# Kernel optimization log

Measured on AMD Instinct MI355X. Metric: run time of the kernel, lower is better.

The kernel has to match this reference:

```python
import jax, jax.numpy as jnp
import numpy as np

B, V, NX, R, D, H = 512, 2, 1024, 64, 512, 8
S, NC, HS = 4, 2, 64           # bc_state_dim, num_controls, state-branch hidden
FIN = S * HS + 128             # fusion input dim (state feats + control feats)


def _ln(x, g, b, eps=1e-5):
    mu = jnp.mean(x, axis=-1, keepdims=True)
    var = jnp.mean((x - mu) ** 2, axis=-1, keepdims=True)
    return (x - mu) * jax.lax.rsqrt(var + eps) * g + b


def setup_inputs() -> dict:
    key = jax.random.key(0)
    ks = iter(jax.random.split(key, 64))
    def rn(shape, s=0.02):
        return jax.random.normal(next(ks), shape, dtype=jnp.float32) * s
    inp = {}
    inp['a_n'] = jax.random.normal(next(ks), (B, V, R), dtype=jnp.float32)
    inp['BC_Ctrl'] = jax.random.normal(next(ks), (B, S + NC), dtype=jnp.float32)
    inp['Phi'] = rn((V, NX, R), 1.0 / np.sqrt(NX).astype(np.float32))
    # per-variable attention params (stacked on leading V axis)
    inp['Wq_w'] = rn((V, 1, D));   inp['Wq_b'] = rn((V, D))
    inp['Wk_w'] = rn((V, NX, D));  inp['Wk_b'] = rn((V, D))
    inp['Wv_w'] = rn((V, NX, D));  inp['Wv_b'] = rn((V, D))
    inp['attn_ow'] = rn((V, D, D)); inp['attn_ob'] = rn((V, D))
    inp['proj_w'] = rn((V, D, 1));  inp['proj_b'] = rn((V, 1))
    # ImprovedUpdateFFN (num_layers=3, hidden=d_model) + LayerNorm
    inp['ffn_w1'] = rn((V, R, D)); inp['ffn_b1'] = rn((V, D))
    inp['ffn_w2'] = rn((V, D, D)); inp['ffn_b2'] = rn((V, D))
    inp['ffn_w3'] = rn((V, D, R)); inp['ffn_b3'] = rn((V, R))
    inp['ffn_ln_g'] = jnp.ones((V, R), jnp.float32)
    inp['ffn_ln_b'] = jnp.zeros((V, R), jnp.float32)
    # a0_mapping: Linear -> ReLU -> LayerNorm
    inp['a0_w'] = rn((V, R, R)); inp['a0_b'] = rn((V, R))
    inp['a0_ln_g'] = jnp.ones((V, R), jnp.float32)
    inp['a0_ln_b'] = jnp.zeros((V, R), jnp.float32)
    inp['alpha'] = jnp.full((V,), 0.1, jnp.float32)
    # UniversalLifting params
    inp['sb_w'] = rn((S, 1, HS)); inp['sb_b'] = rn((S, HS))
    inp['cm_w1'] = rn((NC, 64));  inp['cm_b1'] = rn((64,))
    inp['cm_w2'] = rn((64, 128)); inp['cm_b2'] = rn((128,))
    inp['fu_w1'] = rn((FIN, 256)); inp['fu_b1'] = rn((256,))
    inp['fu_w2'] = rn((256, 512)); inp['fu_b2'] = rn((512,))
    inp['fu_w3'] = rn((512, 256)); inp['fu_b3'] = rn((256,))
    inp['fu_w4'] = rn((256, V * NX)); inp['fu_b4'] = rn((V * NX,))
    return inp


def reference(a_n, BC_Ctrl, Phi, Wq_w, Wq_b, Wk_w, Wk_b, Wv_w, Wv_b,
              attn_ow, attn_ob, proj_w, proj_b,
              ffn_w1, ffn_b1, ffn_w2, ffn_b2, ffn_w3, ffn_b3, ffn_ln_g, ffn_ln_b,
              a0_w, a0_b, a0_ln_g, a0_ln_b, alpha,
              sb_w, sb_b, cm_w1, cm_b1, cm_w2, cm_b2,
              fu_w1, fu_b1, fu_w2, fu_b2, fu_w3, fu_b3, fu_w4, fu_b4):
    gelu = jax.nn.gelu
    # ---- UniversalLifting: U_B [B, V, NX] ----
    bs = BC_Ctrl[:, :S]                                              # [B,S]
    sf = gelu(bs[:, :, None] * sb_w[None, :, 0, :] + sb_b[None])     # [B,S,HS]
    sf = sf.reshape(bs.shape[0], S * HS)
    cf = gelu(BC_Ctrl[:, S:] @ cm_w1 + cm_b1)
    cf = gelu(cf @ cm_w2 + cm_b2)
    f = jnp.concatenate([sf, cf], axis=-1)                           # [B,FIN]
    h = gelu(f @ fu_w1 + fu_b1)
    h = gelu(h @ fu_w2 + fu_b2)
    h = gelu(h @ fu_w3 + fu_b3)
    U_B = (h @ fu_w4 + fu_b4).reshape(-1, V, NX)
    # ---- a0 mapping: Linear -> ReLU -> LayerNorm ----
    a_map = jax.nn.relu(jnp.einsum('bvr,vrs->bvs', a_n, a0_w) + a0_b[None])
    a_map = _ln(a_map, a0_ln_g[None], a0_ln_b[None])                 # [B,V,R]
    # ---- ImprovedUpdateFFN residual update ----
    h1 = gelu(jnp.einsum('bvr,vrd->bvd', a_map, ffn_w1) + ffn_b1[None])
    h2 = gelu(jnp.einsum('bvd,vde->bve', h1, ffn_w2) + ffn_b2[None])
    o = jnp.einsum('bvd,vdr->bvr', h2, ffn_w3) + ffn_b3[None]
    ffn_update = _ln(o + a_map, ffn_ln_g[None], ffn_ln_b[None])      # [B,V,R]
    # ---- Q/K/V; K,V depend only on Phi (batch-independent) ----
    Q = a_map[:, :, :, None] * Wq_w[:, 0][None, :, None, :] + Wq_b[None, :, None, :]  # [B,V,R,D]
    K = jnp.einsum('vnr,vnd->vrd', Phi, Wk_w) + Wk_b[:, None, :]     # [V,R,D]
    Vm = jnp.einsum('vnr,vnd->vrd', Phi, Wv_w) + Wv_b[:, None, :]    # [V,R,D]
    hd = D // H
    Qh = Q.reshape(-1, V, R, H, hd)
    Kh = K.reshape(V, R, H, hd)
    Vh = Vm.reshape(V, R, H, hd)
    # softmax-free linear attention: z = Q (K^T V) per head
    KV = jnp.einsum('vrhk,vrhl->vhkl', Kh, Vh)                        # [V,H,hd,hd]
    z = jnp.einsum('bvrhk,vhkl->bvrhl', Qh, KV).reshape(-1, V, R, D)
    z = jnp.einsum('bvrd,vde->bvre', z, attn_ow) + attn_ob[None, :, None, :]
    z = z / jnp.sqrt(jnp.float32(D))
    a_update = jnp.einsum('bvrd,vdo->bvro', z, proj_w)[..., 0] + proj_b[:, 0][None, :, None]
    a_next = a_map + a_update + alpha[None, :, None] * ffn_update     # [B,V,R]
    U_hat = jnp.einsum('vnr,bvr->bvn', Phi, a_next) + U_B             # [B,V,NX]
    return U_hat
```

## Files before the change

kernel.cpp:

```cpp
#include <hip/hip_runtime.h>
#include <hip/hip_bf16.h>
#include <math.h>


typedef unsigned short ushort_t;
using short8 = __attribute__((ext_vector_type(8))) short;
using f32x4  = __attribute__((ext_vector_type(4))) float;

__device__ __forceinline__ float gelu_f(float x) {
    float x3 = x*x*x;
    return 0.5f*x*(1.0f + tanhf(0.7978845608028654f*(x + 0.044715f*x3)));
}

__device__ __forceinline__ float wave_sum(float x) {
    #pragma unroll
    for (int m = 32; m >= 1; m >>= 1) x += __shfl_xor(x, m, 64);
    return x;
}

__device__ __forceinline__ ushort_t f2bf(float x) {
    unsigned u = __float_as_uint(x);
    unsigned r = (u + 0x7FFFu + ((u >> 16) & 1u)) >> 16;
    return (ushort_t)r;
}
__device__ __forceinline__ float bf2f(ushort_t h) {
    return __uint_as_float(((unsigned)h) << 16);
}

struct Ptrs {
    const float *a_n, *BC, *Phi, *Wq_w, *Wq_b, *Wk_w, *Wk_b, *Wv_w, *Wv_b,
                *attn_ow, *attn_ob, *proj_w, *proj_b,
                *ffn_w3, *ffn_b3, *ffn_ln_g, *ffn_ln_b,
                *a0_w, *a0_b, *a0_ln_g, *a0_ln_b, *alpha,
                *sb_w, *sb_b, *cm_w1, *cm_b1, *cm_w2, *cm_b2,
                *fu_b1, *fu_b2, *fu_b3, *fu_b4, *ffn_b1, *ffn_b2;
    float *opj, *u0, *u1, *u2, *pkq, *pqq, *pvo, *phirs, *bias2, *out;
    ushort_t *amap_bf, *h1_bf, *h2_bf, *fbuf_bf, *hA_bf, *hB_bf;
    ushort_t *w_fu1t, *w_fu2t, *w_fu3t, *w_ffn1t, *w_ffn2t, *w_ffn3t,
             *Abig, *Bbig;
};

struct CvtDesc { const float* src; ushort_t* dst; int K, N, mode, ldd, coff; };
struct CvtArgs { CvtDesc d[12]; int cum[13]; };

__device__ void cvt_dev(char* smem, int tile, const CvtDesc& d, const Ptrs& p)
{
    const int t = threadIdx.x;
    if (d.mode == 2) {
        const int row = t >> 2, q = t & 3;
        const float* s = d.src + (long)(tile*64 + row)*64 + q*16;
        ushort_t* dst  = d.dst + (long)(tile*64 + row)*384 + d.coff + q*16;
        ushort_t* dz   = d.dst + (long)(tile*64 + row)*384 + (64 - d.coff) + q*16;
        float sum = 0.f;
        #pragma unroll
        for (int i = 0; i < 4; ++i) {
            float4 x = *(const float4*)(s + i*4);
            ushort4 w; w.x=f2bf(x.x); w.y=f2bf(x.y); w.z=f2bf(x.z); w.w=f2bf(x.w);
            *(ushort4*)(dst + i*4) = w;
            ushort4 z; z.x=0; z.y=0; z.z=0; z.w=0;
            *(ushort4*)(dz + i*4) = z;
            sum += x.x + x.y + x.z + x.w;
        }
        sum += __shfl_xor(sum, 1, 64);
        sum += __shfl_xor(sum, 2, 64);
        if (q == 0) p.phirs[d.K + tile*64 + row] = sum;
    } else {
        float* tl = (float*)smem;
        const int ntn = d.N >> 5;
        const int kt = tile / ntn, nt = tile % ntn;
        const int r = t >> 3, c0 = (t & 7) * 4;
        float4 v = *(const float4*)(d.src + (long)(kt*32 + r)*d.N + nt*32 + c0);
        tl[r*33 + c0] = v.x; tl[r*33 + c0+1] = v.y;
        tl[r*33 + c0+2] = v.z; tl[r*33 + c0+3] = v.w;
        __syncthreads();
        ushort4 w;
        w.x = f2bf(tl[(c0+0)*33 + r]); w.y = f2bf(tl[(c0+1)*33 + r]);
        w.z = f2bf(tl[(c0+2)*33 + r]); w.w = f2bf(tl[(c0+3)*33 + r]);
        *(ushort4*)(d.dst + (long)(nt*32 + r)*d.ldd + d.coff + kt*32 + c0) = w;
    }
}

__device__ void bgemm_dev(char* smem_,
    const ushort_t* __restrict__ A, const ushort_t* __restrict__ B,
    const float* __restrict__ bias,
    void* __restrict__ Cv, int m0, int n0, int K, int ldc,
    int EPI, bool OUTBF)
{
    ushort_t* lds = (ushort_t*)smem_;
    const int tid = threadIdx.x;
    const int w = tid >> 6, l = tid & 63;
    const int ml = l & 15, kg = l >> 4;
    const int srow = tid >> 2, sslot = tid & 3;
    const ushort_t* Ag = A + (long)(m0 + srow)*K + sslot*8;
    const ushort_t* Bg = B + (long)(n0 + srow)*K + sslot*8;
    auto L = [&](int buf, int ab, int row, int col) {
        return lds + (((buf*2 + ab)*64 + row)*40 + col);
    };
    f32x4 acc[4] = {};
    const int nt = K >> 5;
    int4 ra = *(const int4*)Ag;
    int4 rb = *(const int4*)Bg;
    *(int4*)L(0,0,srow,sslot*8) = ra;
    *(int4*)L(0,1,srow,sslot*8) = rb;
    __syncthreads();
    for (int t = 0; t < nt; ++t) {
        const int cur = t & 1;
        if (t + 1 < nt) {
            ra = *(const int4*)(Ag + (t+1)*32);
            rb = *(const int4*)(Bg + (t+1)*32);
        }
        short8 af = *(const short8*)L(cur,0,w*16 + ml,kg*8);
        #pragma unroll
        for (int f = 0; f < 4; ++f) {
            short8 bfr = *(const short8*)L(cur,1,f*16 + ml,kg*8);
            acc[f] = __builtin_amdgcn_mfma_f32_16x16x32_bf16(af, bfr, acc[f], 0, 0, 0);
        }
        if (t + 1 < nt) {
            *(int4*)L(cur^1,0,srow,sslot*8) = ra;
            *(int4*)L(cur^1,1,srow,sslot*8) = rb;
            __syncthreads();
        }
    }
    float* Cf = (float*)Cv; ushort_t* Cb = (ushort_t*)Cv;
    const int mr = m0 + w*16 + kg*4;
    const int nc = n0 + ml;
    #pragma unroll
    for (int f = 0; f < 4; ++f) {
        const int n = nc + f*16;
        const float bs = bias[n];
        #pragma unroll
        for (int r = 0; r < 4; ++r) {
            float x = acc[f][r] + bs;
            if (EPI == 1) x = gelu_f(x);
            if (OUTBF) Cb[(long)(mr + r)*ldc + n] = f2bf(x);
            else       Cf[(long)(mr + r)*ldc + n] = x;
        }
    }
}

__device__ void control_dev(char* smem, int b, const Ptrs& p)
{
    float* bc  = (float*)smem;
    float* cf1 = bc + 8;
    const int tid = threadIdx.x;
    if (tid < 6) bc[tid] = p.BC[b*6 + tid];
    __syncthreads();
    {
        int s = tid >> 6;
        p.fbuf_bf[(long)b*384 + tid] = f2bf(gelu_f(bc[s]*p.sb_w[tid] + p.sb_b[tid]));
    }
    if (tid < 64) {
        cf1[tid] = gelu_f(bc[4]*p.cm_w1[tid] + bc[5]*p.cm_w1[64+tid] + p.cm_b1[tid]);
    }
    __syncthreads();
    if (tid < 128) {
        float acc = p.cm_b2[tid];
        #pragma unroll 8
        for (int i = 0; i < 64; ++i) acc = fmaf(cf1[i], p.cm_w2[i*128 + tid], acc);
        p.fbuf_bf[(long)b*384 + 256 + tid] = f2bf(gelu_f(acc));
    }
}

__device__ void a_map_dev(char* smem, int bx, int v, const Ptrs& p)
{
    float* arow = (float*)smem;
    const int w = threadIdx.x >> 6, lane = threadIdx.x & 63;
    const int b = bx*4 + w;
    arow[w*64 + lane] = p.a_n[((long)b*2 + v)*64 + lane];
    __syncthreads();
    float acc = p.a0_b[v*64 + lane];
    #pragma unroll 8
    for (int rp = 0; rp < 64; ++rp)
        acc = fmaf(arow[w*64 + rp], p.a0_w[((long)v*64 + rp)*64 + lane], acc);
    float x = fmaxf(acc, 0.0f);
    float mu = wave_sum(x) * (1.0f/64.0f);
    float d = x - mu;
    float var = wave_sum(d*d) * (1.0f/64.0f);
    float y = d * rsqrtf(var + 1e-5f) * p.a0_ln_g[v*64 + lane] + p.a0_ln_b[v*64 + lane];
    p.amap_bf[((long)v*512 + b)*64 + lane] = f2bf(y);
}

__device__ void opj_dev(int oi, const Ptrs& p)
{
    const int tid = threadIdx.x;
    const int v = oi >> 3, dc = oi & 7;
    const int d = dc*64 + (tid >> 2);
    const int e0 = (tid & 3)*128;
    const float* row = p.attn_ow + ((long)v*512 + d)*512 + e0;
    const float* pj  = p.proj_w + v*512 + e0;
    float s = 0.f;
    #pragma unroll 8
    for (int j = 0; j < 128; ++j) s = fmaf(row[j], pj[j], s);
    s += __shfl_xor(s, 1, 64);
    s += __shfl_xor(s, 2, 64);
    if ((tid & 3) == 0) p.opj[v*512 + d] = s;
}

__device__ void u01_dev(int i, const Ptrs& p)
{
    const int tid = threadIdx.x;
    const int w = tid >> 6, lane = tid & 63;
    const int v = i >> 4, c = i & 15;
    const float* wq = p.Wq_w + v*512;
    const float* wb = p.Wq_b + v*512;
    for (int pass = 0; pass < 16; ++pass) {
        const int n = c*64 + pass*4 + w;
        const float* row = p.Wk_w + ((long)v*1024 + n)*512 + lane*8;
        float4 a = *(const float4*)row, b = *(const float4*)(row + 4);
        float s0 = 0.f, s1 = 0.f;
        #pragma unroll
        for (int j = 0; j < 8; ++j) {
            float x = (j < 4) ? ((const float*)&a)[j] : ((const float*)&b)[j-4];
            s0 = fmaf(x, wq[lane*8 + j], s0);
            s1 = fmaf(x, wb[lane*8 + j], s1);
        }
        s0 += __shfl_xor(s0,1,64); s0 += __shfl_xor(s0,2,64); s0 += __shfl_xor(s0,4,64);
        s1 += __shfl_xor(s1,1,64); s1 += __shfl_xor(s1,2,64); s1 += __shfl_xor(s1,4,64);
        if ((lane & 7) == 0) {
            const int h = lane >> 3;
            p.u0[((long)v*1024 + n)*8 + h] = s0;
            p.u1[((long)v*1024 + n)*8 + h] = s1;
        }
    }
}

__device__ void u2_dev(int i, const Ptrs& p)
{
    const int tid = threadIdx.x;
    const int w = tid >> 6, lane = tid & 63;
    const int v = i >> 4, c = i & 15;
    const float* oj = p.opj + v*512;
    for (int pass = 0; pass < 16; ++pass) {
        const int n = c*64 + pass*4 + w;
        const float* row = p.Wv_w + ((long)v*1024 + n)*512 + lane*8;
        float4 a = *(const float4*)row, b = *(const float4*)(row + 4);
        float s0 = 0.f;
        #pragma unroll
        for (int j = 0; j < 8; ++j) {
            float x = (j < 4) ? ((const float*)&a)[j] : ((const float*)&b)[j-4];
            s0 = fmaf(x, oj[lane*8 + j], s0);
        }
        s0 += __shfl_xor(s0,1,64); s0 += __shfl_xor(s0,2,64); s0 += __shfl_xor(s0,4,64);
        if ((lane & 7) == 0) p.u2[((long)v*1024 + n)*8 + (lane >> 3)] = s0;
    }
}

__device__ void kqqq_dev(int i, const Ptrs& p)
{
    const int tid = threadIdx.x;
    const int v = i >> 3, c = i & 7;
    const int r = tid & 63, hp = tid >> 6;
    const int h0 = hp*2, h1 = h0 + 1;
    float k0=0.f,k1=0.f,q0=0.f,q1=0.f;
    const float* Pb = p.Phi + ((long)v*1024 + c*128)*64 + r;
    const float* U0 = p.u0 + ((long)v*1024 + c*128)*8;
    const float* U1 = p.u1 + ((long)v*1024 + c*128)*8;
    #pragma unroll 4
    for (int n = 0; n < 128; ++n) {
        float phi = Pb[(long)n*64];
        k0 = fmaf(phi, U0[n*8+h0], k0); k1 = fmaf(phi, U0[n*8+h1], k1);
        q0 = fmaf(phi, U1[n*8+h0], q0); q1 = fmaf(phi, U1[n*8+h1], q1);
    }
    const long o = (((long)v*8 + c)*64 + r)*8;
    p.pkq[o+h0] = k0; p.pkq[o+h1] = k1;
    p.pqq[o+h0] = q0; p.pqq[o+h1] = q1;
}

__device__ void pvo_dev(int i, const Ptrs& p)
{
    const int tid = threadIdx.x;
    const int v = i >> 3, c = i & 7;
    const int r = tid & 63, hp = tid >> 6;
    const int h0 = hp*2, h1 = h0 + 1;
    float a0 = 0.f, a1 = 0.f;
    const float* Pb = p.Phi + ((long)v*1024 + c*128)*64 + r;
    const float* U2 = p.u2 + ((long)v*1024 + c*128)*8;
    #pragma unroll 4
    for (int n = 0; n < 128; ++n) {
        float phi = Pb[(long)n*64];
        a0 = fmaf(phi, U2[n*8+h0], a0);
        a1 = fmaf(phi, U2[n*8+h1], a1);
    }
    const long o = (((long)v*8 + c)*64 + r)*8;
    p.pvo[o+h0] = a0; p.pvo[o+h1] = a1;
}

__device__ float2 consts_final_dev(char* smem, int v, const Ptrs& p)
{
    const int tid = threadIdx.x;
    const int r = tid & 63, hp = tid >> 6;
    const int h0 = hp*2, h1 = h0 + 1;
    float k0=0.f,k1=0.f,q0=0.f,q1=0.f,w0=0.f,w1=0.f;
    #pragma unroll
    for (int c = 0; c < 8; ++c) {
        const long o = (((long)v*8 + c)*64 + r)*8;
        k0 += p.pkq[o+h0]; k1 += p.pkq[o+h1];
        q0 += p.pqq[o+h0]; q1 += p.pqq[o+h1];
        w0 += p.pvo[o+h0]; w1 += p.pvo[o+h1];
    }
    float bk0=0.f,bk1=0.f,bq0=0.f,bq1=0.f,bv0=0.f,bv1=0.f;
    #pragma unroll 8
    for (int j = 0; j < 64; ++j) {
        float b0 = p.Wk_b[v*512 + h0*64 + j], b1 = p.Wk_b[v*512 + h1*64 + j];
        bk0 = fmaf(b0, p.Wq_w[v*512 + h0*64 + j], bk0);
        bk1 = fmaf(b1, p.Wq_w[v*512 + h1*64 + j], bk1);
        bq0 = fmaf(b0, p.Wq_b[v*512 + h0*64 + j], bq0);
        bq1 = fmaf(b1, p.Wq_b[v*512 + h1*64 + j], bq1);
        float c0v = p.Wv_b[v*512 + h0*64 + j], c1v = p.Wv_b[v*512 + h1*64 + j];
        bv0 = fmaf(c0v, p.opj[v*512 + h0*64 + j], bv0);
        bv1 = fmaf(c1v, p.opj[v*512 + h1*64 + j], bv1);
    }
    w0 += bv0; w1 += bv1;
    k0 += bk0; k1 += bk1; q0 += bq0; q1 += bq1;
    float s1 = k0*w0 + k1*w1;
    float s0 = q0*w0 + q1*w1;
    float sA = p.attn_ob[v*512 + tid]*p.proj_w[v*512 + tid]
             + p.attn_ob[v*512 + 256 + tid]*p.proj_w[v*512 + 256 + tid];
    s1 = wave_sum(s1); s0 = wave_sum(s0); sA = wave_sum(sA);
    float* red = (float*)smem;
    const int w = tid >> 6, l = tid & 63;
    __syncthreads();
    if (l == 0) { red[w] = s1; red[4+w] = s0; red[8+w] = sA; }
    __syncthreads();
    float S1 = red[0]+red[1]+red[2]+red[3];
    float S0 = red[4]+red[5]+red[6]+red[7];
    float SA = red[8]+red[9]+red[10]+red[11];
    __syncthreads();
    const float inv = 0.044194173824159216f;
    float2 res;
    res.x = S1*inv;
    res.y = (S0 + SA)*inv + p.proj_b[v];
    return res;
}

__device__ void ogemm_ln_dev(char* smem_, int v, int m0, const Ptrs& p)
{
    const float c1 = consts_final_dev(smem_, v, p).x;

    ushort_t* lds = (ushort_t*)smem_;
    const int tid = threadIdx.x;
    const int w = tid >> 6, l = tid & 63;
    const int ml = l & 15, kg = l >> 4;
    const int srow = tid >> 2, sslot = tid & 3;
    const ushort_t* A = p.h2_bf + (long)v*262144;
    const ushort_t* B = p.w_ffn3t + (long)v*32768;
    const float* bias = p.ffn_b3 + v*64;
    const ushort_t* Ag = A + (long)(m0 + srow)*512 + sslot*8;
    const ushort_t* Bg = B + (long)srow*512 + sslot*8;
    auto L = [&](int buf, int ab, int row, int col) {
        return lds + (((buf*2 + ab)*64 + row)*40 + col);
    };
    f32x4 acc[4] = {};
    int4 ra = *(const int4*)Ag;
    int4 rb = *(const int4*)Bg;
    *(int4*)L(0,0,srow,sslot*8) = ra;
    *(int4*)L(0,1,srow,sslot*8) = rb;
    __syncthreads();
    for (int t = 0; t < 16; ++t) {
        const int cur = t & 1;
        if (t + 1 < 16) {
            ra = *(const int4*)(Ag + (t+1)*32);
            rb = *(const int4*)(Bg + (t+1)*32);
        }
        short8 af = *(const short8*)L(cur,0,w*16 + ml,kg*8);
        #pragma unroll
        for (int f = 0; f < 4; ++f) {
            short8 bfr = *(const short8*)L(cur,1,f*16 + ml,kg*8);
            acc[f] = __builtin_amdgcn_mfma_f32_16x16x32_bf16(af, bfr, acc[f], 0, 0, 0);
        }
        if (t + 1 < 16) {
            *(int4*)L(cur^1,0,srow,sslot*8) = ra;
            *(int4*)L(cur^1,1,srow,sslot*8) = rb;
            __syncthreads();
        }
    }
    __syncthreads();
    float* ot = (float*)smem_;
    {
        const int rl = w*16 + kg*4;
        #pragma unroll
        for (int f = 0; f < 4; ++f) {
            const int n = ml + f*16;
            const float bs = bias[n];
            #pragma unroll
            for (int r = 0; r < 4; ++r)
                ot[(rl + r)*66 + n] = acc[f][r] + bs;
        }
    }
    __syncthreads();
    const float g  = p.ffn_ln_g[v*64 + l];
    const float bt = p.ffn_ln_b[v*64 + l];
    const float al = p.alpha[v];
    for (int rr = 0; rr < 16; ++rr) {
        const int row = w*16 + rr;
        const int b = m0 + row;
        const float am = bf2f(p.amap_bf[((long)v*512 + b)*64 + l]);
        float t = ot[row*66 + l] + am;
        float mu = wave_sum(t) * (1.0f/64.0f);
        float dd = t - mu;
        float var = wave_sum(dd*dd) * (1.0f/64.0f);
        float u = dd * rsqrtf(var + 1e-5f) * g + bt;
        p.Abig[(long)b*384 + v*64 + l] = f2bf(am*(1.0f + c1) + al*u);
    }
}

__device__ void bias2_dev(char* smem, const Ptrs& p)
{
    const float c00 = consts_final_dev(smem, 0, p).y;
    const float c01 = consts_final_dev(smem, 1, p).y;
    #pragma unroll
    for (int k = 0; k < 8; ++k) {
        const int n2 = k*256 + threadIdx.x;
        const float c0 = (n2 >> 10) ? c01 : c00;
        p.bias2[n2] = p.fu_b4[n2] + c0*p.phirs[n2];
    }
}

__global__ __launch_bounds__(256) void stage0_k(Ptrs p, CvtArgs ca, int ncvt)
{
    extern __shared__ char smem[];
    const int bx = blockIdx.x;
    if (bx < ncvt) {
        int e = 0;
        while (bx >= ca.cum[e+1]) ++e;
        cvt_dev(smem, bx - ca.cum[e], ca.d[e], p);
    } else if (bx < ncvt + 512) {
        control_dev(smem, bx - ncvt, p);
    } else if (bx < ncvt + 768) {
        int i = bx - ncvt - 512;
        a_map_dev(smem, i & 127, i >> 7, p);
    } else if (bx < ncvt + 784) {
        opj_dev(bx - ncvt - 768, p);
    } else {
        u01_dev(bx - ncvt - 784, p);
    }
}

__global__ __launch_bounds__(256) void stage1_k(Ptrs p)
{
    extern __shared__ char smem[];
    const int bx = blockIdx.x;
    if (bx < 32) {
        bgemm_dev(smem, p.fbuf_bf, p.w_fu1t, p.fu_b1, p.hA_bf,
                  (bx>>2)*64, (bx&3)*64, 384, 256, 1, true);
    } else if (bx < 160) {
        int i = bx - 32; int v = i >> 6; i &= 63;
        bgemm_dev(smem, p.amap_bf + (long)v*32768, p.w_ffn1t + (long)v*32768,
                  p.ffn_b1 + v*512, (void*)(p.h1_bf + (long)v*262144),
                  (i>>3)*64, (i&7)*64, 64, 512, 1, true);
    } else if (bx < 192) {
        u2_dev(bx - 160, p);
    } else {
        kqqq_dev(bx - 192, p);
    }
}

__global__ __launch_bounds__(256) void stage2_k(Ptrs p)
{
    extern __shared__ char smem[];
    const int bx = blockIdx.x;
    if (bx < 64) {
        bgemm_dev(smem, p.hA_bf, p.w_fu2t, p.fu_b2, p.hB_bf,
                  (bx>>3)*64, (bx&7)*64, 256, 512, 1, true);
    } else if (bx < 192) {
        int i = bx - 64; int v = i >> 6; i &= 63;
        bgemm_dev(smem, p.h1_bf + (long)v*262144, p.w_ffn2t + (long)v*262144,
                  p.ffn_b2 + v*512, (void*)(p.h2_bf + (long)v*262144),
                  (i>>3)*64, (i&7)*64, 512, 512, 1, true);
    } else {
        pvo_dev(bx - 192, p);
    }
}

__global__ __launch_bounds__(256) void stage3_k(Ptrs p)
{
    extern __shared__ char smem[];
    const int bx = blockIdx.x;
    if (bx < 32) {
        bgemm_dev(smem, p.hB_bf, p.w_fu3t, p.fu_b3, (void*)(p.Abig + 128),
                  (bx>>2)*64, (bx&3)*64, 512, 384, 1, true);
    } else if (bx < 48) {
        int i = bx - 32;
        ogemm_ln_dev(smem, i >> 3, (i & 7)*64, p);
    } else {
        bias2_dev(smem, p);
    }
}

__global__ __launch_bounds__(256) void stage4_k(Ptrs p)
{
    extern __shared__ char smem[];
    const int bx = blockIdx.x;
    bgemm_dev(smem, p.Abig, p.Bbig, p.bias2, (void*)p.out,
              (bx>>5)*64, (bx&31)*64, 384, 2048, 0, false);
}

extern "C" void kernel_launch(void* const* d_in, const int* in_sizes, int n_in,
                              void* d_out, int out_size, void* d_ws, size_t ws_size,
                              hipStream_t stream)
{
    const float* a_n      = (const float*)d_in[0];
    const float* BC       = (const float*)d_in[1];
    const float* Phi      = (const float*)d_in[2];
    const float* Wq_w     = (const float*)d_in[3];
    const float* Wq_b     = (const float*)d_in[4];
    const float* Wk_w     = (const float*)d_in[5];
    const float* Wk_b     = (const float*)d_in[6];
    const float* Wv_w     = (const float*)d_in[7];
    const float* Wv_b     = (const float*)d_in[8];
    const float* attn_ow  = (const float*)d_in[9];
    const float* attn_ob  = (const float*)d_in[10];
    const float* proj_w   = (const float*)d_in[11];
    const float* proj_b   = (const float*)d_in[12];
    const float* ffn_w1   = (const float*)d_in[13];
    const float* ffn_b1   = (const float*)d_in[14];
    const float* ffn_w2   = (const float*)d_in[15];
    const float* ffn_b2   = (const float*)d_in[16];
    const float* ffn_w3   = (const float*)d_in[17];
    const float* ffn_b3   = (const float*)d_in[18];
    const float* ffn_ln_g = (const float*)d_in[19];
    const float* ffn_ln_b = (const float*)d_in[20];
    const float* a0_w     = (const float*)d_in[21];
    const float* a0_b     = (const float*)d_in[22];
    const float* a0_ln_g  = (const float*)d_in[23];
    const float* a0_ln_b  = (const float*)d_in[24];
    const float* alpha    = (const float*)d_in[25];
    const float* sb_w     = (const float*)d_in[26];
    const float* sb_b     = (const float*)d_in[27];
    const float* cm_w1    = (const float*)d_in[28];
    const float* cm_b1    = (const float*)d_in[29];
    const float* cm_w2    = (const float*)d_in[30];
    const float* cm_b2    = (const float*)d_in[31];
    const float* fu_w1    = (const float*)d_in[32];
    const float* fu_b1    = (const float*)d_in[33];
    const float* fu_w2    = (const float*)d_in[34];
    const float* fu_b2    = (const float*)d_in[35];
    const float* fu_w3    = (const float*)d_in[36];
    const float* fu_b3    = (const float*)d_in[37];
    const float* fu_w4    = (const float*)d_in[38];
    const float* fu_b4    = (const float*)d_in[39];

    float* ws = (float*)d_ws;
    Ptrs p;
    p.a_n = a_n; p.BC = BC; p.Phi = Phi; p.Wq_w = Wq_w; p.Wq_b = Wq_b;
    p.Wk_w = Wk_w; p.Wk_b = Wk_b; p.Wv_w = Wv_w; p.Wv_b = Wv_b;
    p.attn_ow = attn_ow; p.attn_ob = attn_ob; p.proj_w = proj_w; p.proj_b = proj_b;
    p.ffn_w3 = ffn_w3; p.ffn_b3 = ffn_b3; p.ffn_ln_g = ffn_ln_g; p.ffn_ln_b = ffn_ln_b;
    p.a0_w = a0_w; p.a0_b = a0_b; p.a0_ln_g = a0_ln_g; p.a0_ln_b = a0_ln_b;
    p.alpha = alpha; p.sb_w = sb_w; p.sb_b = sb_b;
    p.cm_w1 = cm_w1; p.cm_b1 = cm_b1; p.cm_w2 = cm_w2; p.cm_b2 = cm_b2;
    p.fu_b1 = fu_b1; p.fu_b2 = fu_b2; p.fu_b3 = fu_b3; p.fu_b4 = fu_b4;
    p.ffn_b1 = ffn_b1; p.ffn_b2 = ffn_b2;

    p.opj     = ws;
    p.u0      = ws + 1024;
    p.u1      = ws + 17408;
    p.u2      = ws + 33792;
    p.pkq     = ws + 50176;
    p.pqq     = ws + 58368;
    p.pvo     = ws + 66560;
    p.phirs   = ws + 74752;
    p.bias2   = ws + 76800;
    p.amap_bf = (ushort_t*)(ws + 78848);
    p.h1_bf   = (ushort_t*)(ws + 111616);
    p.h2_bf   = (ushort_t*)(ws + 373760);
    p.fbuf_bf = (ushort_t*)(ws + 635904);
    p.hA_bf   = (ushort_t*)(ws + 734208);
    p.hB_bf   = (ushort_t*)(ws + 799744);
    p.w_fu1t  = (ushort_t*)(ws + 930816);
    p.w_fu2t  = (ushort_t*)(ws + 979968);
    p.w_fu3t  = (ushort_t*)(ws + 1045504);
    p.w_ffn1t = (ushort_t*)(ws + 1111040);
    p.w_ffn2t = (ushort_t*)(ws + 1143808);
    p.w_ffn3t = (ushort_t*)(ws + 1405952);
    p.Abig    = (ushort_t*)(ws + 1438720);
    p.Bbig    = (ushort_t*)(ws + 1537024);
    p.out     = (float*)d_out;

    CvtArgs ca;
    auto set = [&](int i, const float* s, ushort_t* dst, int K, int N,
                   int mode, int ldd, int coff) {
        ca.d[i].src = s; ca.d[i].dst = dst; ca.d[i].K = K; ca.d[i].N = N;
        ca.d[i].mode = mode; ca.d[i].ldd = ldd; ca.d[i].coff = coff;
    };
    set(0,  fu_w1,           p.w_fu1t,           384, 256,  0, 384, 0);
    set(1,  fu_w2,           p.w_fu2t,           256, 512,  0, 256, 0);
    set(2,  fu_w3,           p.w_fu3t,           512, 256,  0, 512, 0);
    set(3,  fu_w4,           p.Bbig,             256, 2048, 0, 384, 128);
    set(4,  ffn_w1,          p.w_ffn1t,          64,  512,  0, 64,  0);
    set(5,  ffn_w1 + 32768,  p.w_ffn1t + 32768,  64,  512,  0, 64,  0);
    set(6,  ffn_w2,          p.w_ffn2t,          512, 512,  0, 512, 0);
    set(7,  ffn_w2 + 262144, p.w_ffn2t + 262144, 512, 512,  0, 512, 0);
    set(8,  Phi,             p.Bbig,             0,    0,   2, 384, 0);
    set(9,  Phi + 65536,     p.Bbig + (long)1024*384, 1024, 0, 2, 384, 64);
    set(10, ffn_w3,          p.w_ffn3t,          512, 64,   0, 512, 0);
    set(11, ffn_w3 + 32768,  p.w_ffn3t + 32768,  512, 64,   0, 512, 0);
    const int tl[12] = {96,128,128,512,32,32,256,256,16,16,32,32};
    ca.cum[0] = 0;
    for (int i = 0; i < 12; ++i) ca.cum[i+1] = ca.cum[i] + tl[i];
    const int ncvt = ca.cum[12];

    stage0_k<<<ncvt + 816, 256, 4352,  stream>>>(p, ca, ncvt);
    stage1_k<<<208,        256, 20480, stream>>>(p);
    stage2_k<<<208,        256, 20480, stream>>>(p);
    stage3_k<<<49,         256, 20480, stream>>>(p);
    stage4_k<<<256,        256, 20480, stream>>>(p);
}
```

Baseline: 75.06 us.

## Convert fp32 weights to bf16 inside GEMM tile loads, drop pre-conversion pass

Removes the stage-0 pass that transposed and converted every fp32 weight matrix to bf16 in workspace. The GEMMs now read the fp32 weights directly, convert to bf16 and write them transposed into LDS during tile staging. Stage 4 now splits its K loop between a pre-converted Phi block and on-the-fly fu_w4 tiles. This avoids a full extra read and write of the weights and frees many stage-0 blocks. The cost is twice the global bytes for B tiles and scalar, strided LDS stores that may cause bank conflicts in every GEMM tile, plus redundant conversion across M-tiles.

```diff
diff --git a/kernel.cpp b/kernel.cpp
--- a/kernel.cpp
+++ b/kernel.cpp
@@ -30,84 +30,77 @@
 struct Ptrs {
     const float *a_n, *BC, *Phi, *Wq_w, *Wq_b, *Wk_w, *Wk_b, *Wv_w, *Wv_b,
                 *attn_ow, *attn_ob, *proj_w, *proj_b,
-                *ffn_w3, *ffn_b3, *ffn_ln_g, *ffn_ln_b,
+                *ffn_w1, *ffn_w2, *ffn_w3, *ffn_b3, *ffn_ln_g, *ffn_ln_b,
                 *a0_w, *a0_b, *a0_ln_g, *a0_ln_b, *alpha,
                 *sb_w, *sb_b, *cm_w1, *cm_b1, *cm_w2, *cm_b2,
+                *fu_w1, *fu_w2, *fu_w3, *fu_w4,
                 *fu_b1, *fu_b2, *fu_b3, *fu_b4, *ffn_b1, *ffn_b2;
     float *opj, *u0, *u1, *u2, *pkq, *pqq, *pvo, *phirs, *bias2, *out;
-    ushort_t *amap_bf, *h1_bf, *h2_bf, *fbuf_bf, *hA_bf, *hB_bf;
-    ushort_t *w_fu1t, *w_fu2t, *w_fu3t, *w_ffn1t, *w_ffn2t, *w_ffn3t,
-             *Abig, *Bbig;
+    ushort_t *amap_bf, *h1_bf, *h2_bf, *fbuf_bf, *hA_bf, *hB_bf, *Abig, *Bphi;
 };
 
-struct CvtDesc { const float* src; ushort_t* dst; int K, N, mode, ldd, coff; };
-struct CvtArgs { CvtDesc d[12]; int cum[13]; };
-
-__device__ void cvt_dev(char* smem, int tile, const CvtDesc& d, const Ptrs& p)
+struct CvtDesc { const float* src; ushort_t* dst; int K, ldd, coff; };
+struct CvtArgs { CvtDesc d[4]; int cum[5]; };
+
+__device__ void cvt_dev(int tile, const CvtDesc& d, const Ptrs& p)
 {
     const int t = threadIdx.x;
-    if (d.mode == 2) {
-        const int row = t >> 2, q = t & 3;
-        const float* s = d.src + (long)(tile*64 + row)*64 + q*16;
-        ushort_t* dst  = d.dst + (long)(tile*64 + row)*384 + d.coff + q*16;
-        ushort_t* dz   = d.dst + (long)(tile*64 + row)*384 + (64 - d.coff) + q*16;
-        float sum = 0.f;
-        #pragma unroll
-        for (int i = 0; i < 4; ++i) {
-            float4 x = *(const float4*)(s + i*4);
-            ushort4 w; w.x=f2bf(x.x); w.y=f2bf(x.y); w.z=f2bf(x.z); w.w=f2bf(x.w);
-            *(ushort4*)(dst + i*4) = w;
-            ushort4 z; z.x=0; z.y=0; z.z=0; z.w=0;
-            *(ushort4*)(dz + i*4) = z;
-            sum += x.x + x.y + x.z + x.w;
-        }
-        sum += __shfl_xor(sum, 1, 64);
-        sum += __shfl_xor(sum, 2, 64);
-        if (q == 0) p.phirs[d.K + tile*64 + row] = sum;
-    } else {
-        float* tl = (float*)smem;
-        const int ntn = d.N >> 5;
-        const int kt = tile / ntn, nt = tile % ntn;
-        const int r = t >> 3, c0 = (t & 7) * 4;
-        float4 v = *(const float4*)(d.src + (long)(kt*32 + r)*d.N + nt*32 + c0);
-        tl[r*33 + c0] = v.x; tl[r*33 + c0+1] = v.y;
-        tl[r*33 + c0+2] = v.z; tl[r*33 + c0+3] = v.w;
-        __syncthreads();
-        ushort4 w;
-        w.x = f2bf(tl[(c0+0)*33 + r]); w.y = f2bf(tl[(c0+1)*33 + r]);
-        w.z = f2bf(tl[(c0+2)*33 + r]); w.w = f2bf(tl[(c0+3)*33 + r]);
-        *(ushort4*)(d.dst + (long)(nt*32 + r)*d.ldd + d.coff + kt*32 + c0) = w;
-    }
-}
-
-__device__ void bgemm_dev(char* smem_,
-    const ushort_t* __restrict__ A, const ushort_t* __restrict__ B,
-    const float* __restrict__ bias,
-    void* __restrict__ Cv, int m0, int n0, int K, int ldc,
-    int EPI, bool OUTBF)
+    const int row = t >> 2, q = t & 3;
+    const float* s = d.src + (long)(tile*64 + row)*64 + q*16;
+    ushort_t* dst  = d.dst + (long)(tile*64 + row)*d.ldd + d.coff + q*16;
+    ushort_t* dz   = d.dst + (long)(tile*64 + row)*d.ldd + (64 - d.coff) + q*16;
+    float sum = 0.f;
+    #pragma unroll
+    for (int i = 0; i < 4; ++i) {
+        float4 x = *(const float4*)(s + i*4);
+        ushort4 w; w.x=f2bf(x.x); w.y=f2bf(x.y); w.z=f2bf(x.z); w.w=f2bf(x.w);
+        *(ushort4*)(dst + i*4) = w;
+        ushort4 z; z.x=0; z.y=0; z.z=0; z.w=0;
+        *(ushort4*)(dz + i*4) = z;
+        sum += x.x + x.y + x.z + x.w;
+    }
+    sum += __shfl_xor(sum, 1, 64);
+    sum += __shfl_xor(sum, 2, 64);
+    if (q == 0) p.phirs[d.K + tile*64 + row] = sum;
+}
+
+__device__ void bgemm_f32b_dev(char* smem_,
+    const ushort_t* __restrict__ A, const float* __restrict__ Bf,
+    const float* __restrict__ bias, void* __restrict__ Cv,
+    int m0, int n0, int K, int ldb, int ldc, int EPI, bool OUTBF)
 {
     ushort_t* lds = (ushort_t*)smem_;
     const int tid = threadIdx.x;
     const int w = tid >> 6, l = tid & 63;
     const int ml = l & 15, kg = l >> 4;
     const int srow = tid >> 2, sslot = tid & 3;
+    const int kk = tid >> 3, ng = (tid & 7)*8;
     const ushort_t* Ag = A + (long)(m0 + srow)*K + sslot*8;
-    const ushort_t* Bg = B + (long)(n0 + srow)*K + sslot*8;
+    const float* Bg = Bf + n0 + ng;
     auto L = [&](int buf, int ab, int row, int col) {
         return lds + (((buf*2 + ab)*64 + row)*40 + col);
+    };
+    auto wrB = [&](int buf, float4 b0, float4 b1) {
+        ushort_t* bs = L(buf, 1, 0, 0);
+        bs[(ng+0)*40 + kk] = f2bf(b0.x); bs[(ng+1)*40 + kk] = f2bf(b0.y);
+        bs[(ng+2)*40 + kk] = f2bf(b0.z); bs[(ng+3)*40 + kk] = f2bf(b0.w);
+        bs[(ng+4)*40 + kk] = f2bf(b1.x); bs[(ng+5)*40 + kk] = f2bf(b1.y);
+        bs[(ng+6)*40 + kk] = f2bf(b1.z); bs[(ng+7)*40 + kk] = f2bf(b1.w);
     };
     f32x4 acc[4] = {};
     const int nt = K >> 5;
     int4 ra = *(const int4*)Ag;
-    int4 rb = *(const int4*)Bg;
+    float4 rb0 = *(const float4*)(Bg + (long)kk*ldb);
+    float4 rb1 = *(const float4*)(Bg + (long)kk*ldb + 4);
     *(int4*)L(0,0,srow,sslot*8) = ra;
-    *(int4*)L(0,1,srow,sslot*8) = rb;
+    wrB(0, rb0, rb1);
     __syncthreads();
     for (int t = 0; t < nt; ++t) {
         const int cur = t & 1;
         if (t + 1 < nt) {
-            ra = *(const int4*)(Ag + (t+1)*32);
-            rb = *(const int4*)(Bg + (t+1)*32);
+            ra  = *(const int4*)(Ag + (t+1)*32);
+            rb0 = *(const float4*)(Bg + (long)((t+1)*32 + kk)*ldb);
+            rb1 = *(const float4*)(Bg + (long)((t+1)*32 + kk)*ldb + 4);
         }
         short8 af = *(const short8*)L(cur,0,w*16 + ml,kg*8);
         #pragma unroll
@@ -117,7 +110,7 @@
         }
         if (t + 1 < nt) {
             *(int4*)L(cur^1,0,srow,sslot*8) = ra;
-            *(int4*)L(cur^1,1,srow,sslot*8) = rb;
+            wrB(cur^1, rb0, rb1);
             __syncthreads();
         }
     }
@@ -342,25 +335,34 @@
     const int w = tid >> 6, l = tid & 63;
     const int ml = l & 15, kg = l >> 4;
     const int srow = tid >> 2, sslot = tid & 3;
+    const int kk = tid >> 3, ng = (tid & 7)*8;
     const ushort_t* A = p.h2_bf + (long)v*262144;
-    const ushort_t* B = p.w_ffn3t + (long)v*32768;
+    const float* Bf = p.ffn_w3 + (long)v*32768;
     const float* bias = p.ffn_b3 + v*64;
     const ushort_t* Ag = A + (long)(m0 + srow)*512 + sslot*8;
-    const ushort_t* Bg = B + (long)srow*512 + sslot*8;
     auto L = [&](int buf, int ab, int row, int col) {
         return lds + (((buf*2 + ab)*64 + row)*40 + col);
     };
+    auto wrB = [&](int buf, float4 b0, float4 b1) {
+        ushort_t* bs = L(buf, 1, 0, 0);
+        bs[(ng+0)*40 + kk] = f2bf(b0.x); bs[(ng+1)*40 + kk] = f2bf(b0.y);
+        bs[(ng+2)*40 + kk] = f2bf(b0.z); bs[(ng+3)*40 + kk] = f2bf(b0.w);
+        bs[(ng+4)*40 + kk] = f2bf(b1.x); bs[(ng+5)*40 + kk] = f2bf(b1.y);
+        bs[(ng+6)*40 + kk] = f2bf(b1.z); bs[(ng+7)*40 + kk] = f2bf(b1.w);
+    };
     f32x4 acc[4] = {};
     int4 ra = *(const int4*)Ag;
-    int4 rb = *(const int4*)Bg;
+    float4 rb0 = *(const float4*)(Bf + (long)kk*64 + ng);
+    float4 rb1 = *(const float4*)(Bf + (long)kk*64 + ng + 4);
     *(int4*)L(0,0,srow,sslot*8) = ra;
-    *(int4*)L(0,1,srow,sslot*8) = rb;
+    wrB(0, rb0, rb1);
     __syncthreads();
     for (int t = 0; t < 16; ++t) {
         const int cur = t & 1;
         if (t + 1 < 16) {
-            ra = *(const int4*)(Ag + (t+1)*32);
-            rb = *(const int4*)(Bg + (t+1)*32);
+            ra  = *(const int4*)(Ag + (t+1)*32);
+            rb0 = *(const float4*)(Bf + (long)((t+1)*32 + kk)*64 + ng);
+            rb1 = *(const float4*)(Bf + (long)((t+1)*32 + kk)*64 + ng + 4);
         }
         short8 af = *(const short8*)L(cur,0,w*16 + ml,kg*8);
         #pragma unroll
@@ -370,7 +372,7 @@
         }
         if (t + 1 < 16) {
             *(int4*)L(cur^1,0,srow,sslot*8) = ra;
-            *(int4*)L(cur^1,1,srow,sslot*8) = rb;
+            wrB(cur^1, rb0, rb1);
             __syncthreads();
         }
     }
@@ -423,7 +425,7 @@
     if (bx < ncvt) {
         int e = 0;
         while (bx >= ca.cum[e+1]) ++e;
-        cvt_dev(smem, bx - ca.cum[e], ca.d[e], p);
+        cvt_dev(bx - ca.cum[e], ca.d[e], p);
     } else if (bx < ncvt + 512) {
         control_dev(smem, bx - ncvt, p);
     } else if (bx < ncvt + 768) {
@@ -441,13 +443,13 @@
     extern __shared__ char smem[];
     const int bx = blockIdx.x;
     if (bx < 32) {
-        bgemm_dev(smem, p.fbuf_bf, p.w_fu1t, p.fu_b1, p.hA_bf,
-                  (bx>>2)*64, (bx&3)*64, 384, 256, 1, true);
+        bgemm_f32b_dev(smem, p.fbuf_bf, p.fu_w1, p.fu_b1, p.hA_bf,
+                       (bx>>2)*64, (bx&3)*64, 384, 256, 256, 1, true);
     } else if (bx < 160) {
         int i = bx - 32; int v = i >> 6; i &= 63;
-        bgemm_dev(smem, p.amap_bf + (long)v*32768, p.w_ffn1t + (long)v*32768,
-                  p.ffn_b1 + v*512, (void*)(p.h1_bf + (long)v*262144),
-                  (i>>3)*64, (i&7)*64, 64, 512, 1, true);
+        bgemm_f32b_dev(smem, p.amap_bf + (long)v*32768, p.ffn_w1 + (long)v*32768,
+                       p.ffn_b1 + v*512, (void*)(p.h1_bf + (long)v*262144),
+                       (i>>3)*64, (i&7)*64, 64, 512, 512, 1, true);
     } else if (bx < 192) {
         u2_dev(bx - 160, p);
     } else {
@@ -460,13 +462,13 @@
     extern __shared__ char smem[];
     const int bx = blockIdx.x;
     if (bx < 64) {
-        bgemm_dev(smem, p.hA_bf, p.w_fu2t, p.fu_b2, p.hB_bf,
-                  (bx>>3)*64, (bx&7)*64, 256, 512, 1, true);
+        bgemm_f32b_dev(smem, p.hA_bf, p.fu_w2, p.fu_b2, p.hB_bf,
+                       (bx>>3)*64, (bx&7)*64, 256, 512, 512, 1, true);
     } else if (bx < 192) {
         int i = bx - 64; int v = i >> 6; i &= 63;
-        bgemm_dev(smem, p.h1_bf + (long)v*262144, p.w_ffn2t + (long)v*262144,
-                  p.ffn_b2 + v*512, (void*)(p.h2_bf + (long)v*262144),
-                  (i>>3)*64, (i&7)*64, 512, 512, 1, true);
+        bgemm_f32b_dev(smem, p.h1_bf + (long)v*262144, p.ffn_w2 + (long)v*262144,
+                       p.ffn_b2 + v*512, (void*)(p.h2_bf + (long)v*262144),
+                       (i>>3)*64, (i&7)*64, 512, 512, 512, 1, true);
     } else {
         pvo_dev(bx - 192, p);
     }
@@ -477,8 +479,8 @@
     extern __shared__ char smem[];
     const int bx = blockIdx.x;
     if (bx < 32) {
-        bgemm_dev(smem, p.hB_bf, p.w_fu3t, p.fu_b3, (void*)(p.Abig + 128),
-                  (bx>>2)*64, (bx&3)*64, 512, 384, 1, true);
+        bgemm_f32b_dev(smem, p.hB_bf, p.fu_w3, p.fu_b3, (void*)(p.Abig + 128),
+                       (bx>>2)*64, (bx&3)*64, 512, 256, 384, 1, true);
     } else if (bx < 48) {
         int i = bx - 32;
         ogemm_ln_dev(smem, i >> 3, (i & 7)*64, p);
@@ -490,9 +492,68 @@
 __global__ __launch_bounds__(256) void stage4_k(Ptrs p)
 {
     extern __shared__ char smem[];
+    ushort_t* lds = (ushort_t*)smem;
     const int bx = blockIdx.x;
-    bgemm_dev(smem, p.Abig, p.Bbig, p.bias2, (void*)p.out,
-              (bx>>5)*64, (bx&31)*64, 384, 2048, 0, false);
+    const int m0 = (bx >> 5)*64, n0 = (bx & 31)*64;
+    const int tid = threadIdx.x;
+    const int w = tid >> 6, l = tid & 63;
+    const int ml = l & 15, kg = l >> 4;
+    const int srow = tid >> 2, sslot = tid & 3;
+    const int kk = tid >> 3, ng = (tid & 7)*8;
+    const ushort_t* Ag = p.Abig + (long)(m0 + srow)*384 + sslot*8;
+    const ushort_t* Bp = p.Bphi + (long)(n0 + srow)*128 + sslot*8;
+    const float* Wf = p.fu_w4 + n0 + ng;
+    auto L = [&](int buf, int ab, int row, int col) {
+        return lds + (((buf*2 + ab)*64 + row)*40 + col);
+    };
+    auto wrB = [&](int buf, float4 b0, float4 b1) {
+        ushort_t* bs = L(buf, 1, 0, 0);
+        bs[(ng+0)*40 + kk] = f2bf(b0.x); bs[(ng+1)*40 + kk] = f2bf(b0.y);
+        bs[(ng+2)*40 + kk] = f2bf(b0.z); bs[(ng+3)*40 + kk] = f2bf(b0.w);
+        bs[(ng+4)*40 + kk] = f2bf(b1.x); bs[(ng+5)*40 + kk] = f2bf(b1.y);
+        bs[(ng+6)*40 + kk] = f2bf(b1.z); bs[(ng+7)*40 + kk] = f2bf(b1.w);
+    };
+    f32x4 acc[4] = {};
+    int4 ra = *(const int4*)Ag;
+    int4 rbi = *(const int4*)Bp;
+    float4 rb0, rb1;
+    *(int4*)L(0,0,srow,sslot*8) = ra;
+    *(int4*)L(0,1,srow,sslot*8) = rbi;
+    __syncthreads();
+    for (int t = 0; t < 12; ++t) {
+        const int cur = t & 1;
+        if (t + 1 < 12) {
+            ra = *(const int4*)(Ag + (t+1)*32);
+            if (t + 1 < 4) {
+                rbi = *(const int4*)(Bp + (t+1)*32);
+            } else {
+                rb0 = *(const float4*)(Wf + (long)((t+1)*32 - 128 + kk)*2048);
+                rb1 = *(const float4*)(Wf + (long)((t+1)*32 - 128 + kk)*2048 + 4);
+            }
+        }
+        short8 af = *(const short8*)L(cur,0,w*16 + ml,kg*8);
+        #pragma unroll
+        for (int f = 0; f < 4; ++f) {
+            short8 bfr = *(const short8*)L(cur,1,f*16 + ml,kg*8);
+            acc[f] = __builtin_amdgcn_mfma_f32_16x16x32_bf16(af, bfr, acc[f], 0, 0, 0);
+        }
+        if (t + 1 < 12) {
+            *(int4*)L(cur^1,0,srow,sslot*8) = ra;
+            if (t + 1 < 4) *(int4*)L(cur^1,1,srow,sslot*8) = rbi;
+            else           wrB(cur^1, rb0, rb1);
+            __syncthreads();
+        }
+    }
+    const int mr = m0 + w*16 + kg*4;
+    const int nc = n0 + ml;
+    #pragma unroll
+    for (int f = 0; f < 4; ++f) {
+        const int n = nc + f*16;
+        const float bs = p.bias2[n];
+        #pragma unroll
+        for (int r = 0; r < 4; ++r)
+            p.out[(long)(mr + r)*2048 + n] = acc[f][r] + bs;
+    }
 }
 
 extern "C" void kernel_launch(void* const* d_in, const int* in_sizes, int n_in,
@@ -545,10 +606,12 @@
     p.a_n = a_n; p.BC = BC; p.Phi = Phi; p.Wq_w = Wq_w; p.Wq_b = Wq_b;
     p.Wk_w = Wk_w; p.Wk_b = Wk_b; p.Wv_w = Wv_w; p.Wv_b = Wv_b;
     p.attn_ow = attn_ow; p.attn_ob = attn_ob; p.proj_w = proj_w; p.proj_b = proj_b;
-    p.ffn_w3 = ffn_w3; p.ffn_b3 = ffn_b3; p.ffn_ln_g = ffn_ln_g; p.ffn_ln_b = ffn_ln_b;
+    p.ffn_w1 = ffn_w1; p.ffn_w2 = ffn_w2; p.ffn_w3 = ffn_w3; p.ffn_b3 = ffn_b3;
+    p.ffn_ln_g = ffn_ln_g; p.ffn_ln_b = ffn_ln_b;
     p.a0_w = a0_w; p.a0_b = a0_b; p.a0_ln_g = a0_ln_g; p.a0_ln_b = a0_ln_b;
     p.alpha = alpha; p.sb_w = sb_w; p.sb_b = sb_b;
     p.cm_w1 = cm_w1; p.cm_b1 = cm_b1; p.cm_w2 = cm_w2; p.cm_b2 = cm_b2;
+    p.fu_w1 = fu_w1; p.fu_w2 = fu_w2; p.fu_w3 = fu_w3; p.fu_w4 = fu_w4;
     p.fu_b1 = fu_b1; p.fu_b2 = fu_b2; p.fu_b3 = fu_b3; p.fu_b4 = fu_b4;
     p.ffn_b1 = ffn_b1; p.ffn_b2 = ffn_b2;
 
@@ -567,38 +630,17 @@
     p.fbuf_bf = (ushort_t*)(ws + 635904);
     p.hA_bf   = (ushort_t*)(ws + 734208);
     p.hB_bf   = (ushort_t*)(ws + 799744);
-    p.w_fu1t  = (ushort_t*)(ws + 930816);
-    p.w_fu2t  = (ushort_t*)(ws + 979968);
-    p.w_fu3t  = (ushort_t*)(ws + 1045504);
-    p.w_ffn1t = (ushort_t*)(ws + 1111040);
-    p.w_ffn2t = (ushort_t*)(ws + 1143808);
-    p.w_ffn3t = (ushort_t*)(ws + 1405952);
-    p.Abig    = (ushort_t*)(ws + 1438720);
-    p.Bbig    = (ushort_t*)(ws + 1537024);
+    p.Abig    = (ushort_t*)(ws + 930816);
+    p.Bphi    = (ushort_t*)(ws + 1029120);
     p.out     = (float*)d_out;
 
     CvtArgs ca;
-    auto set = [&](int i, const float* s, ushort_t* dst, int K, int N,
-                   int mode, int ldd, int coff) {
-        ca.d[i].src = s; ca.d[i].dst = dst; ca.d[i].K = K; ca.d[i].N = N;
-        ca.d[i].mode = mode; ca.d[i].ldd = ldd; ca.d[i].coff = coff;
-    };
-    set(0,  fu_w1,           p.w_fu1t,           384, 256,  0, 384, 0);
-    set(1,  fu_w2,           p.w_fu2t,           256, 512,  0, 256, 0);
-    set(2,  fu_w3,           p.w_fu3t,           512, 256,  0, 512, 0);
-    set(3,  fu_w4,           p.Bbig,             256, 2048, 0, 384, 128);
-    set(4,  ffn_w1,          p.w_ffn1t,          64,  512,  0, 64,  0);
-    set(5,  ffn_w1 + 32768,  p.w_ffn1t + 32768,  64,  512,  0, 64,  0);
-    set(6,  ffn_w2,          p.w_ffn2t,          512, 512,  0, 512, 0);
-    set(7,  ffn_w2 + 262144, p.w_ffn2t + 262144, 512, 512,  0, 512, 0);
-    set(8,  Phi,             p.Bbig,             0,    0,   2, 384, 0);
-    set(9,  Phi + 65536,     p.Bbig + (long)1024*384, 1024, 0, 2, 384, 64);
-    set(10, ffn_w3,          p.w_ffn3t,          512, 64,   0, 512, 0);
-    set(11, ffn_w3 + 32768,  p.w_ffn3t + 32768,  512, 64,   0, 512, 0);
-    const int tl[12] = {96,128,128,512,32,32,256,256,16,16,32,32};
-    ca.cum[0] = 0;
-    for (int i = 0; i < 12; ++i) ca.cum[i+1] = ca.cum[i] + tl[i];
-    const int ncvt = ca.cum[12];
+    ca.d[0].src = Phi;          ca.d[0].dst = p.Bphi;
+    ca.d[0].K = 0;    ca.d[0].ldd = 128; ca.d[0].coff = 0;
+    ca.d[1].src = Phi + 65536;  ca.d[1].dst = p.Bphi + (long)1024*128;
+    ca.d[1].K = 1024; ca.d[1].ldd = 128; ca.d[1].coff = 64;
+    ca.cum[0] = 0; ca.cum[1] = 16; ca.cum[2] = 32;
+    const int ncvt = 32;
 
     stage0_k<<<ncvt + 816, 256, 4352,  stream>>>(p, ca, ncvt);
     stage1_k<<<208,        256, 20480, stream>>>(p);
```

New measurement: 80.35 us. 7.1% more time.
